# Performance work log

Measured on AMD Instinct MI355X. Metric: run time of the kernel, lower is better.

Reference implementation:

```python
import jax, jax.numpy as jnp
import numpy as np
import itertools

DIM, ORDER = 8, 4  # matches init_kwargs

def _exponent_table(dim, order):
    # All multisets (non-decreasing tuples) of size 0..order over range(dim),
    # sorted lexicographically -- identical to sorted(Counter keys) in the torch code
    # (Counter keys are sorted tuples; combinations_with_replacement yields exactly those).
    terms = sorted(itertools.chain.from_iterable(
        itertools.combinations_with_replacement(range(dim), o) for o in range(order + 1)))
    E = np.zeros((len(terms), dim), dtype=np.int32)
    for i, t in enumerate(terms):
        for d in t:
            E[i, d] += 1
    return E

E = jnp.asarray(_exponent_table(DIM, ORDER))  # [nterms=495, dim=8]


def setup_inputs() -> dict:
    key = jax.random.key(0)
    x = jax.random.normal(key, (65536, DIM), dtype=jnp.float32)
    return {"x": x}


def reference(x):
    # torch: cat_i prod_d x[..., d] ** ind_i.count(d)
    # vectorized: broadcast pow with exponent table, reduce-product over dim axis
    # x: [B, dim] -> [B, 1, dim] ** [nterms, dim] -> prod over dim -> [B, nterms]
    return jnp.prod(x[..., None, :] ** E, axis=-1)
```

## Files before the change

kernel.cpp:

```cpp
#include <hip/hip_runtime.h>


struct Specs {
    unsigned short uv[64][8];
    unsigned short pp[64];
};

constexpr int pidx_c(int a, int b) {
    return 9 + 8 * a - (a * (a - 1)) / 2 + (b - a);
}

constexpr Specs make_specs() {
    Specs S{};
    for (int l = 0; l < 64; ++l) {
        int s1 = 0, s2 = 0, u1 = 0, u2 = 0;
        if (l >= 1 && l <= 8) { s1 = l - 1; u1 = 1; }
        else if (l >= 9 && l < 45) {
            int k = l - 9, i = 0;
            while (k >= 8 - i) { k -= 8 - i; ++i; }
            s1 = i; s2 = i + k; u1 = 1; u2 = 1;
        }
        S.pp[l] = (unsigned short)(s1 | (s2 << 4) | (u1 << 8) | (u2 << 9));
    }
    int idx = 1;
    for (int a = 0; a < 8; ++a) {
        S.uv[idx & 63][idx >> 6] = (unsigned short)(1 + a); ++idx;
        for (int b = a; b < 8; ++b) {
            S.uv[idx & 63][idx >> 6] = (unsigned short)pidx_c(a, b); ++idx;
            for (int c = b; c < 8; ++c) {
                S.uv[idx & 63][idx >> 6] =
                    (unsigned short)(pidx_c(a, b) | ((1 + c) << 8)); ++idx;
                for (int d = c; d < 8; ++d) {
                    S.uv[idx & 63][idx >> 6] =
                        (unsigned short)(pidx_c(a, b) | (pidx_c(c, d) << 8));
                    ++idx;
                }
            }
        }
    }
    return S;
}

__constant__ Specs SPECS = make_specs();

#define WAVES_PER_BLOCK 4
#define ROWS_PER_WAVE   8
#define ROWS_PER_BLOCK  (WAVES_PER_BLOCK * ROWS_PER_WAVE)

__global__ __launch_bounds__(256, 8) void TotalDegree_29755533426739_kernel(
    const float* __restrict__ x, float* __restrict__ out, int B) {
    __shared__ float xs[ROWS_PER_BLOCK * 8];

    const int tid  = (int)threadIdx.x;
    const int lane = tid & 63;
    const int wid  = tid >> 6;

    {
        const int gi = (int)blockIdx.x * (ROWS_PER_BLOCK * 8) + tid;
        xs[tid] = (gi < B * 8) ? x[gi] : 0.0f;
    }

    const int ppv  = (int)SPECS.pp[lane];
    const int s1   = ppv & 15;
    const int s2   = (ppv >> 4) & 15;
    const bool use1 = ((ppv >> 8) & 1) != 0;
    const bool use2 = ((ppv >> 9) & 1) != 0;

    int u4[8], v4[8];
    #pragma unroll
    for (int c = 0; c < 8; ++c) {
        const int sp = (int)SPECS.uv[lane][c];
        u4[c] = (sp & 255) << 2;
        v4[c] = (sp >> 8) << 2;
    }

    __syncthreads();

    const float* xw = xs + wid * (ROWS_PER_WAVE * 8);
    const unsigned baseRow =
        (unsigned)blockIdx.x * ROWS_PER_BLOCK + (unsigned)(wid * ROWS_PER_WAVE);
    unsigned off = baseRow * 495u + (unsigned)lane;

    #pragma unroll 2
    for (int rr = 0; rr < ROWS_PER_WAVE; ++rr) {
        const float a1 = xw[rr * 8 + s1];
        const float a2 = xw[rr * 8 + s2];
        const float P  = (use1 ? a1 : 1.0f) * (use2 ? a2 : 1.0f);
        const int  Pi  = __float_as_int(P);

        #pragma unroll
        for (int c = 0; c < 8; ++c) {
            const float f1 = __int_as_float(__builtin_amdgcn_ds_bpermute(u4[c], Pi));
            const float f2 = __int_as_float(__builtin_amdgcn_ds_bpermute(v4[c], Pi));
            const float tv = f1 * f2;
            if (c < 7) {
                out[off + (unsigned)(c * 64)] = tv;
            } else if (lane < 47) {
                out[off + 448u] = tv;
            }
        }
        off += 495u;
    }
}

extern "C" void kernel_launch(void* const* d_in, const int* in_sizes, int n_in,
                              void* d_out, int out_size, void* d_ws, size_t ws_size,
                              hipStream_t stream) {
    const float* x = (const float*)d_in[0];
    float* out = (float*)d_out;
    const int B = in_sizes[0] / 8;
    const int grid = (B + ROWS_PER_BLOCK - 1) / ROWS_PER_BLOCK;
    hipLaunchKernelGGL(TotalDegree_29755533426739_kernel,
                       dim3(grid), dim3(256), 0, stream, x, out, B);
}
```

Measured before the change: 130.5 us.

## Stage partial products in LDS and emit 16-byte nontemporal vector stores

```diff
diff --git a/kernel.cpp b/kernel.cpp
--- a/kernel.cpp
+++ b/kernel.cpp
@@ -1,8 +1,10 @@
 #include <hip/hip_runtime.h>
 
 
-struct Specs {
-    unsigned short uv[64][8];
+typedef float f32x4 __attribute__((ext_vector_type(4)));
+
+struct Tbl {
+    unsigned short e[64][8][4];
     unsigned short pp[64];
 };
 
@@ -10,8 +12,33 @@
     return 9 + 8 * a - (a * (a - 1)) / 2 + (b - a);
 }
 
-constexpr Specs make_specs() {
-    Specs S{};
+constexpr Tbl make_tbl() {
+    Tbl T{};
+    unsigned short lin[512] = {};
+    int idx = 1;
+    for (int a = 0; a < 8; ++a) {
+        lin[idx++] = (unsigned short)(1 + a);
+        for (int b = a; b < 8; ++b) {
+            lin[idx++] = (unsigned short)pidx_c(a, b);
+            for (int c = b; c < 8; ++c) {
+                lin[idx++] = (unsigned short)(pidx_c(a, b) | ((1 + c) << 8));
+                for (int d = c; d < 8; ++d)
+                    lin[idx++] = (unsigned short)(pidx_c(a, b) | (pidx_c(c, d) << 8));
+            }
+        }
+    }
+    for (int l = 0; l < 64; ++l)
+        for (int c = 0; c < 8; ++c)
+            for (int k = 0; k < 4; ++k) {
+                int ei = c * 256 + 4 * l + k;
+                if (ei < 1980) {
+                    int r = ei / 495, t = ei % 495;
+                    int u = lin[t] & 255, v = lin[t] >> 8;
+                    T.e[l][c][k] = (unsigned short)((r * 64 + u) | ((r * 64 + v) << 8));
+                } else {
+                    T.e[l][c][k] = 0;
+                }
+            }
     for (int l = 0; l < 64; ++l) {
         int s1 = 0, s2 = 0, u1 = 0, u2 = 0;
         if (l >= 1 && l <= 8) { s1 = l - 1; u1 = 1; }
@@ -20,28 +47,12 @@
             while (k >= 8 - i) { k -= 8 - i; ++i; }
             s1 = i; s2 = i + k; u1 = 1; u2 = 1;
         }
-        S.pp[l] = (unsigned short)(s1 | (s2 << 4) | (u1 << 8) | (u2 << 9));
+        T.pp[l] = (unsigned short)(s1 | (s2 << 4) | (u1 << 8) | (u2 << 9));
     }
-    int idx = 1;
-    for (int a = 0; a < 8; ++a) {
-        S.uv[idx & 63][idx >> 6] = (unsigned short)(1 + a); ++idx;
-        for (int b = a; b < 8; ++b) {
-            S.uv[idx & 63][idx >> 6] = (unsigned short)pidx_c(a, b); ++idx;
-            for (int c = b; c < 8; ++c) {
-                S.uv[idx & 63][idx >> 6] =
-                    (unsigned short)(pidx_c(a, b) | ((1 + c) << 8)); ++idx;
-                for (int d = c; d < 8; ++d) {
-                    S.uv[idx & 63][idx >> 6] =
-                        (unsigned short)(pidx_c(a, b) | (pidx_c(c, d) << 8));
-                    ++idx;
-                }
-            }
-        }
-    }
-    return S;
+    return T;
 }
 
-__constant__ Specs SPECS = make_specs();
+__constant__ Tbl TBL = make_tbl();
 
 #define WAVES_PER_BLOCK 4
 #define ROWS_PER_WAVE   8
@@ -50,6 +61,7 @@
 __global__ __launch_bounds__(256, 8) void TotalDegree_29755533426739_kernel(
     const float* __restrict__ x, float* __restrict__ out, int B) {
     __shared__ float xs[ROWS_PER_BLOCK * 8];
+    __shared__ float Pl[WAVES_PER_BLOCK][256];
 
     const int tid  = (int)threadIdx.x;
     const int lane = tid & 63;
@@ -60,46 +72,51 @@
         xs[tid] = (gi < B * 8) ? x[gi] : 0.0f;
     }
 
-    const int ppv  = (int)SPECS.pp[lane];
+    const int ppv  = (int)TBL.pp[lane];
     const int s1   = ppv & 15;
     const int s2   = (ppv >> 4) & 15;
     const bool use1 = ((ppv >> 8) & 1) != 0;
     const bool use2 = ((ppv >> 9) & 1) != 0;
 
-    int u4[8], v4[8];
+    unsigned long long tw[8];
     #pragma unroll
-    for (int c = 0; c < 8; ++c) {
-        const int sp = (int)SPECS.uv[lane][c];
-        u4[c] = (sp & 255) << 2;
-        v4[c] = (sp >> 8) << 2;
-    }
+    for (int c = 0; c < 8; ++c)
+        tw[c] = *reinterpret_cast<const unsigned long long*>(&TBL.e[lane][c][0]);
 
     __syncthreads();
 
     const float* xw = xs + wid * (ROWS_PER_WAVE * 8);
-    const unsigned baseRow =
+    float* Pw = Pl[wid];
+    const unsigned rowBase =
         (unsigned)blockIdx.x * ROWS_PER_BLOCK + (unsigned)(wid * ROWS_PER_WAVE);
-    unsigned off = baseRow * 495u + (unsigned)lane;
 
-    #pragma unroll 2
-    for (int rr = 0; rr < ROWS_PER_WAVE; ++rr) {
-        const float a1 = xw[rr * 8 + s1];
-        const float a2 = xw[rr * 8 + s2];
-        const float P  = (use1 ? a1 : 1.0f) * (use2 ? a2 : 1.0f);
-        const int  Pi  = __float_as_int(P);
+    #pragma unroll
+    for (int g = 0; g < 2; ++g) {
+        #pragma unroll
+        for (int r = 0; r < 4; ++r) {
+            const float a1 = xw[(g * 4 + r) * 8 + s1];
+            const float a2 = xw[(g * 4 + r) * 8 + s2];
+            Pw[r * 64 + lane] = (use1 ? a1 : 1.0f) * (use2 ? a2 : 1.0f);
+        }
+
+        float* o = out + (rowBase + (unsigned)(g * 4)) * 495u;
+        f32x4* ob = reinterpret_cast<f32x4*>(o) + lane;
 
         #pragma unroll
         for (int c = 0; c < 8; ++c) {
-            const float f1 = __int_as_float(__builtin_amdgcn_ds_bpermute(u4[c], Pi));
-            const float f2 = __int_as_float(__builtin_amdgcn_ds_bpermute(v4[c], Pi));
-            const float tv = f1 * f2;
+            const unsigned w0 = (unsigned)tw[c];
+            const unsigned w1 = (unsigned)(tw[c] >> 32);
+            f32x4 v;
+            v.x = Pw[w0 & 255] * Pw[(w0 >> 8) & 255];
+            v.y = Pw[(w0 >> 16) & 255] * Pw[w0 >> 24];
+            v.z = Pw[w1 & 255] * Pw[(w1 >> 8) & 255];
+            v.w = Pw[(w1 >> 16) & 255] * Pw[w1 >> 24];
             if (c < 7) {
-                out[off + (unsigned)(c * 64)] = tv;
+                __builtin_nontemporal_store(v, ob + c * 64);
             } else if (lane < 47) {
-                out[off + 448u] = tv;
+                __builtin_nontemporal_store(v, ob + 448);
             }
         }
-        off += 495u;
     }
 }
 
```

Result: slower. 163.4 us (+25.2%).
